# Kernel tuning notes

Hardware: AMD Instinct MI355X
Metric: run time of the kernel (lower is better)

Reference implementation:

```python
import jax, jax.numpy as jnp
import numpy as np

K = 3
PAD = 1
K2 = K * K


def _deform_conv(x, offset, w, b):
    """torchvision-style DeformConv2d, stride=1, padding=1, kernel=3, dilation=1.
    x: [B,C,H,W]; offset: [B,2*K2,H,W] (per-tap (dy,dx) interleaved); w: [O,C,K,K]; b: [O].
    """
    B, C, H, W = x.shape
    # kernel tap offsets relative to center (padding=1 => taps at -1,0,1)
    ky = (jnp.arange(K) - PAD).astype(x.dtype)
    kx = (jnp.arange(K) - PAD).astype(x.dtype)
    ky = jnp.repeat(ky, K)   # [K2]
    kx = jnp.tile(kx, K)     # [K2]

    off = offset.reshape(B, K2, 2, H, W)
    # sampling coordinates: [B,K2,H,W]
    yy = off[:, :, 0] + ky[None, :, None, None] + jnp.arange(H, dtype=x.dtype)[None, None, :, None]
    xx = off[:, :, 1] + kx[None, :, None, None] + jnp.arange(W, dtype=x.dtype)[None, None, None, :]

    def sample_one(img, yb, xb):  # img [C,H,W]; yb,xb [K2,H,W]
        y0 = jnp.floor(yb)
        x0 = jnp.floor(xb)
        dy = yb - y0
        dx = xb - x0
        y0i = y0.astype(jnp.int32)
        x0i = x0.astype(jnp.int32)
        img_flat = img.reshape(C, -1)

        def gather(yi, xi):
            valid = (yi >= 0) & (yi < H) & (xi >= 0) & (xi < W)
            idx = jnp.clip(yi, 0, H - 1) * W + jnp.clip(xi, 0, W - 1)
            v = jnp.take(img_flat, idx.reshape(-1), axis=1).reshape(C, K2, H, W)
            return v * valid[None].astype(img.dtype)

        v00 = gather(y0i, x0i)
        v01 = gather(y0i, x0i + 1)
        v10 = gather(y0i + 1, x0i)
        v11 = gather(y0i + 1, x0i + 1)
        w00 = ((1 - dy) * (1 - dx))[None]
        w01 = ((1 - dy) * dx)[None]
        w10 = (dy * (1 - dx))[None]
        w11 = (dy * dx)[None]
        return v00 * w00 + v01 * w01 + v10 * w10 + v11 * w11  # [C,K2,H,W]

    samp = jax.vmap(sample_one)(x, yy, xx)  # [B,C,K2,H,W]
    wr = w.reshape(w.shape[0], C, K2)       # [O,C,K2]
    out = jnp.einsum('bckhw,ock->bohw', samp, wr)
    return out + b[None, :, None, None]


def setup_inputs() -> dict:
    key = jax.random.key(0)
    ks = jax.random.split(key, 8)
    B, Cin, H, W = 16, 256, 32, 32
    Ch, NC = 256, 1000
    fan1 = Cin * K2
    fan2 = Ch * K2
    return {
        'x': jax.random.normal(ks[0], (B, Cin, H, W), jnp.float32),
        'offset': jax.random.normal(ks[1], (B, 2 * K2, H, W), jnp.float32),
        'w1': jax.random.normal(ks[2], (Ch, Cin, K, K), jnp.float32) / np.sqrt(fan1),
        'b1': jnp.zeros((Ch,), jnp.float32),
        'w2': jax.random.normal(ks[3], (Ch, Ch, K, K), jnp.float32) / np.sqrt(fan2),
        'b2': jnp.zeros((Ch,), jnp.float32),
        'fc_w': jax.random.normal(ks[4], (NC, Ch), jnp.float32) / np.sqrt(Ch),
        'fc_b': jnp.zeros((NC,), jnp.float32),
    }


def reference(x, offset, w1, b1, w2, b2, fc_w, fc_b):
    h = jax.nn.relu(_deform_conv(x, offset, w1, b1))
    h = jax.nn.relu(_deform_conv(h, offset, w2, b2))
    pooled = h.mean(axis=(2, 3))            # adaptive_avg_pool2d to (1,1) then flatten
    return pooled @ fc_w.T + fc_b
```

## Files before the change

kernel.cpp:

```cpp
#include <hip/hip_runtime.h>

#define B_   16
#define C_   256
#define H_   32
#define W_   32
#define O_   256
#define K2_  9
#define HW_  1024
#define KTOT 2304
#define NPOS 16384

typedef __bf16 bf16;
typedef __attribute__((ext_vector_type(8))) __bf16 bf16x8;
typedef __attribute__((ext_vector_type(4))) float  f32x4;

__device__ __forceinline__ void gload_lds16(const bf16* g, bf16* l) {
    __builtin_amdgcn_global_load_lds(
        (const __attribute__((address_space(1))) void*)g,
        (__attribute__((address_space(3))) void*)l, 16, 0, 0);
}

__device__ __forceinline__ float4 load4(const float* p, int t) {
    return ((const float4*)p)[t];
}
__device__ __forceinline__ float4 load4(const bf16* p, int t) {
    const ushort4 u = ((const ushort4*)p)[t];
    float4 f;
    f.x = __uint_as_float((unsigned)u.x << 16);
    f.y = __uint_as_float((unsigned)u.y << 16);
    f.z = __uint_as_float((unsigned)u.z << 16);
    f.w = __uint_as_float((unsigned)u.w << 16);
    return f;
}

__global__ __launch_bounds__(256) void prep_w(
    const float* __restrict__ w, bf16* __restrict__ Wm)
{
    const int o = blockIdx.x;
    for (int k = threadIdx.x; k < KTOT; k += 256) {
        const int cg  = k / 72;
        const int rem = k - cg * 72;
        const int tap = rem >> 3;
        const int cl  = rem & 7;
        const int c   = cg * 8 + cl;
        const int chunk  = cg * 9 + tap;
        const int chunkp = (chunk & ~7) | ((chunk ^ o) & 7);
        Wm[(size_t)o * KTOT + chunkp * 8 + cl] =
            (bf16)w[((size_t)o * C_ + c) * K2_ + tap];
    }
}

template<typename T>
__global__ __launch_bounds__(256) void sample_kernel(
    const T* __restrict__ src, size_t c_stride, size_t b_stride,
    const float* __restrict__ off,
    bf16* __restrict__ S)
{
    __shared__ ushort4 midx[576];
    __shared__ float4  mwgt[576];
    __shared__ float4  xs4[2][1152];

    const int tid = threadIdx.x;
    const int bx  = blockIdx.x;
    const int cg  = bx & 31;
    const int rt  = (bx >> 5) & 15;
    const int b   = bx >> 9;
    const int yrow = rt * 2;

    for (int item = tid; item < 576; item += 256) {
        const int pos = item & 63;
        const int k   = item >> 6;
        const int y   = yrow + (pos >> 5);
        const int x   = pos & 31;
        const float dyo = off[((b * 18 + 2 * k)     << 10) + (y << 5) + x];
        const float dxo = off[((b * 18 + 2 * k + 1) << 10) + (y << 5) + x];
        const float yy = dyo + (float)(k / 3 - 1) + (float)y;
        const float xx = dxo + (float)(k % 3 - 1) + (float)x;
        const float fy0 = floorf(yy), fx0 = floorf(xx);
        const float dy = yy - fy0, dx = xx - fx0;
        const int iy0 = (int)fy0, ix0 = (int)fx0;
        const int iy1 = iy0 + 1,  ix1 = ix0 + 1;
        const bool vy0 = (iy0 >= 0) && (iy0 < H_);
        const bool vy1 = (iy1 >= 0) && (iy1 < H_);
        const bool vx0 = (ix0 >= 0) && (ix0 < W_);
        const bool vx1 = (ix1 >= 0) && (ix1 < W_);
        const int cy0 = min(max(iy0, 0), H_ - 1), cy1 = min(max(iy1, 0), H_ - 1);
        const int cx0 = min(max(ix0, 0), W_ - 1), cx1 = min(max(ix1, 0), W_ - 1);
        ushort4 id; float4 wv;
        id.x = (unsigned short)(cy0 * W_ + cx0);
        wv.x = (vy0 && vx0) ? (1.f - dy) * (1.f - dx) : 0.f;
        id.y = (unsigned short)(cy0 * W_ + cx1);
        wv.y = (vy0 && vx1) ? (1.f - dy) * dx         : 0.f;
        id.z = (unsigned short)(cy1 * W_ + cx0);
        wv.z = (vy1 && vx0) ? dy * (1.f - dx)         : 0.f;
        id.w = (unsigned short)(cy1 * W_ + cx1);
        wv.w = (vy1 && vx1) ? dy * dx                 : 0.f;
        midx[item] = id;
        mwgt[item] = wv;
    }

    #pragma unroll
    for (int h = 0; h < 2; ++h) {
        const T* base = src + b * b_stride + (size_t)(cg * 8 + h * 4) * c_stride;
        const float4 v0 = load4(base,                tid);
        const float4 v1 = load4(base + c_stride,     tid);
        const float4 v2 = load4(base + 2 * c_stride, tid);
        const float4 v3 = load4(base + 3 * c_stride, tid);
        const int p0 = 4 * tid;
        xs4[h][(p0    ) + ((p0    ) >> 3)] = make_float4(v0.x, v1.x, v2.x, v3.x);
        xs4[h][(p0 + 1) + ((p0 + 1) >> 3)] = make_float4(v0.y, v1.y, v2.y, v3.y);
        xs4[h][(p0 + 2) + ((p0 + 2) >> 3)] = make_float4(v0.z, v1.z, v2.z, v3.z);
        xs4[h][(p0 + 3) + ((p0 + 3) >> 3)] = make_float4(v0.w, v1.w, v2.w, v3.w);
    }
    __syncthreads();

    for (int item = tid; item < 576; item += 256) {
        const int pos = item & 63;
        const int tap = item >> 6;
        const ushort4 id = midx[item];
        const float4  wv = mwgt[item];
        const int s0 = id.x + (id.x >> 3);
        const int s1 = id.y + (id.y >> 3);
        const int s2 = id.z + (id.z >> 3);
        const int s3 = id.w + (id.w >> 3);
        bf16x8 v;
        #pragma unroll
        for (int h = 0; h < 2; ++h) {
            const float4 a = xs4[h][s0], bb = xs4[h][s1];
            const float4 c = xs4[h][s2], d  = xs4[h][s3];
            v[h * 4 + 0] = (bf16)(wv.x * a.x + wv.y * bb.x + wv.z * c.x + wv.w * d.x);
            v[h * 4 + 1] = (bf16)(wv.x * a.y + wv.y * bb.y + wv.z * c.y + wv.w * d.y);
            v[h * 4 + 2] = (bf16)(wv.x * a.z + wv.y * bb.z + wv.z * c.z + wv.w * d.z);
            v[h * 4 + 3] = (bf16)(wv.x * a.w + wv.y * bb.w + wv.z * c.w + wv.w * d.w);
        }
        const int chunk  = cg * 9 + tap;
        const int chunkp = (chunk & ~7) | ((chunk ^ pos) & 7);
        *(bf16x8*)(S + (size_t)(b * 1024 + rt * 64 + pos) * KTOT + chunkp * 8) = v;
    }
}

template<bool POOL>
__global__ __launch_bounds__(256) void gemm_kernel(
    const bf16* __restrict__ A,
    const bf16* __restrict__ Bm,
    const float* __restrict__ bias,
    bf16* __restrict__ F,
    float* __restrict__ pooled)
{
    __shared__ bf16 Al[128 * 64];
    __shared__ bf16 Bl[64 * 64];

    const int tid  = threadIdx.x;
    const int om   = blockIdx.x >> 8;
    const int pn   = blockIdx.x & 255;
    const int wave = tid >> 6, lane = tid & 63;
    const int wr   = wave >> 1, wc = wave & 1;
    const int l15  = lane & 15, l4 = lane >> 4;

    f32x4 acc[4][2];
    #pragma unroll
    for (int m = 0; m < 4; ++m)
        #pragma unroll
        for (int n = 0; n < 2; ++n) acc[m][n] = (f32x4)0.f;

    for (int kt = 0; kt < KTOT / 64; ++kt) {
        __syncthreads();
        const int k0 = kt * 64;
        #pragma unroll
        for (int i = 0; i < 4; ++i) {
            const int flat = i * 256 + tid;
            const int rr = flat >> 3, kk = (flat & 7) << 3;
            gload_lds16(A + (size_t)(om * 128 + rr) * KTOT + k0 + kk,
                        &Al[(i * 256 + wave * 64) * 8]);
        }
        #pragma unroll
        for (int i = 0; i < 2; ++i) {
            const int flat = i * 256 + tid;
            const int rr = flat >> 3, kk = (flat & 7) << 3;
            gload_lds16(Bm + (size_t)(pn * 64 + rr) * KTOT + k0 + kk,
                        &Bl[(i * 256 + wave * 64) * 8]);
        }
        __syncthreads();

        #pragma unroll
        for (int ks = 0; ks < 2; ++ks) {
            const int cbase = ks * 4 + l4;
            bf16x8 af[4], bq[2];
            #pragma unroll
            for (int m = 0; m < 4; ++m) {
                const int R = wr * 64 + m * 16 + l15;
                af[m] = *(const bf16x8*)&Al[R * 64 + ((cbase ^ R) & 7) * 8];
            }
            #pragma unroll
            for (int n = 0; n < 2; ++n) {
                const int R = wc * 32 + n * 16 + l15;
                bq[n] = *(const bf16x8*)&Bl[R * 64 + ((cbase ^ R) & 7) * 8];
            }
            #pragma unroll
            for (int m = 0; m < 4; ++m)
                #pragma unroll
                for (int n = 0; n < 2; ++n)
                    acc[m][n] = __builtin_amdgcn_mfma_f32_16x16x32_bf16(
                        af[m], bq[n], acc[m][n], 0, 0, 0);
        }
    }

    const int obase = om * 128 + wr * 64;
    if (!POOL) {
        #pragma unroll
        for (int m = 0; m < 4; ++m)
            #pragma unroll
            for (int j = 0; j < 4; ++j) {
                const int o  = obase + m * 16 + l4 * 4 + j;
                const float bb = bias[o];
                #pragma unroll
                for (int n = 0; n < 2; ++n) {
                    const int col = pn * 64 + wc * 32 + n * 16 + l15;
                    F[(size_t)o * NPOS + col] =
                        (bf16)fmaxf(acc[m][n][j] + bb, 0.f);
                }
            }
    } else {
        const int b = pn >> 4;
        #pragma unroll
        for (int m = 0; m < 4; ++m)
            #pragma unroll
            for (int j = 0; j < 4; ++j) {
                const int o  = obase + m * 16 + l4 * 4 + j;
                const float bb = bias[o];
                float s = fmaxf(acc[m][0][j] + bb, 0.f) +
                          fmaxf(acc[m][1][j] + bb, 0.f);
                s += __shfl_xor(s, 1);
                s += __shfl_xor(s, 2);
                s += __shfl_xor(s, 4);
                s += __shfl_xor(s, 8);
                if (l15 == 0)
                    atomicAdd(&pooled[b * 256 + o], s * (1.f / 1024.f));
            }
    }
}

__global__ __launch_bounds__(256) void fc_kernel(
    const float* __restrict__ pooled, const float* __restrict__ fw,
    const float* __restrict__ fb, float* __restrict__ out)
{
    __shared__ float pl[C_];
    const int b = blockIdx.x >> 2;
    const int q = blockIdx.x & 3;
    const int t = threadIdx.x;
    pl[t] = pooled[b * C_ + t];
    __syncthreads();
    const int n = q * 250 + t;
    if (t < 250) {
        const float4* wr = (const float4*)(fw + (size_t)n * C_);
        float s = 0.f;
        #pragma unroll 8
        for (int j = 0; j < C_ / 4; ++j) {
            const float4 v = wr[j];
            s += v.x * pl[4 * j] + v.y * pl[4 * j + 1] +
                 v.z * pl[4 * j + 2] + v.w * pl[4 * j + 3];
        }
        out[b * 1000 + n] = s + fb[n];
    }
}

extern "C" void kernel_launch(void* const* d_in, const int* in_sizes, int n_in,
                              void* d_out, int out_size, void* d_ws, size_t ws_size,
                              hipStream_t stream)
{
    const float* x   = (const float*)d_in[0];
    const float* off = (const float*)d_in[1];
    const float* w1  = (const float*)d_in[2];
    const float* b1  = (const float*)d_in[3];
    const float* w2  = (const float*)d_in[4];
    const float* b2  = (const float*)d_in[5];
    const float* fcw = (const float*)d_in[6];
    const float* fcb = (const float*)d_in[7];
    float* outp = (float*)d_out;

    bf16*  S      = (bf16*)d_ws;
    bf16*  F2     = S + (size_t)NPOS * KTOT;
    bf16*  Wm1    = F2 + (size_t)O_ * NPOS;
    bf16*  Wm2    = Wm1 + (size_t)O_ * KTOT;
    float* pooled = (float*)(Wm2 + (size_t)O_ * KTOT);

    prep_w<<<O_, 256, 0, stream>>>(w1, Wm1);
    prep_w<<<O_, 256, 0, stream>>>(w2, Wm2);
    hipMemsetAsync(pooled, 0, B_ * O_ * sizeof(float), stream);

    sample_kernel<float><<<8192, 256, 0, stream>>>(
        x, (size_t)HW_, (size_t)C_ * HW_, off, S);
    gemm_kernel<false><<<512, 256, 0, stream>>>(Wm1, S, b1, F2, nullptr);

    sample_kernel<bf16><<<8192, 256, 0, stream>>>(
        F2, (size_t)NPOS, (size_t)HW_, off, S);
    gemm_kernel<true><<<512, 256, 0, stream>>>(Wm2, S, b2, nullptr, pooled);

    fc_kernel<<<B_ * 4, 256, 0, stream>>>(pooled, fcw, fcb, outp);
}
```

Before: 242.4 us.

## Use chunk-major tiled layouts for im2col and weights; sample four row tiles per block

The weight matrix and the sampled im2col buffer are now stored chunk-major within each GEMM tile. Each GEMM k-step therefore loads one contiguous 16KB/8KB block and reads LDS without XOR swizzling. The sampling kernel now covers four row tiles per block instead of one, so each 8-channel plane is staged in LDS once per four tiles. The bilinear index and weight computation moves inline, so it is recomputed per channel group rather than cached in LDS. The unswizzled LDS reads may cause bank conflicts, and the larger sample blocks lower the grid size and the available parallelism.

```diff
diff --git a/kernel.cpp b/kernel.cpp
--- a/kernel.cpp
+++ b/kernel.cpp
@@ -1,14 +1,16 @@
 #include <hip/hip_runtime.h>
 
-#define B_   16
-#define C_   256
-#define H_   32
-#define W_   32
-#define O_   256
-#define K2_  9
-#define HW_  1024
-#define KTOT 2304
-#define NPOS 16384
+#define B_     16
+#define C_     256
+#define H_     32
+#define W_     32
+#define O_     256
+#define K2_    9
+#define HW_    1024
+#define KTOT   2304
+#define NPOS   16384
+#define NCHUNK 288
+#define NT     256
 
 typedef __bf16 bf16;
 typedef __attribute__((ext_vector_type(8))) __bf16 bf16x8;
@@ -34,18 +36,18 @@
 }
 
 __global__ __launch_bounds__(256) void prep_w(
-    const float* __restrict__ w, bf16* __restrict__ Wm)
-{
-    const int o = blockIdx.x;
+    const float* __restrict__ w, bf16* __restrict__ Wt)
+{
+    const int o    = blockIdx.x;
+    const int om   = o >> 7, o128 = o & 127;
     for (int k = threadIdx.x; k < KTOT; k += 256) {
         const int cg  = k / 72;
         const int rem = k - cg * 72;
         const int tap = rem >> 3;
         const int cl  = rem & 7;
         const int c   = cg * 8 + cl;
-        const int chunk  = cg * 9 + tap;
-        const int chunkp = (chunk & ~7) | ((chunk ^ o) & 7);
-        Wm[(size_t)o * KTOT + chunkp * 8 + cl] =
+        const int chunk = cg * 9 + tap;
+        Wt[(((size_t)om * NCHUNK + chunk) * 128 + o128) * 8 + cl] =
             (bf16)w[((size_t)o * C_ + c) * K2_ + tap];
     }
 }
@@ -56,48 +58,12 @@
     const float* __restrict__ off,
     bf16* __restrict__ S)
 {
-    __shared__ ushort4 midx[576];
-    __shared__ float4  mwgt[576];
-    __shared__ float4  xs4[2][1152];
+    __shared__ float4 xs4[2][1152];
 
     const int tid = threadIdx.x;
-    const int bx  = blockIdx.x;
-    const int cg  = bx & 31;
-    const int rt  = (bx >> 5) & 15;
-    const int b   = bx >> 9;
-    const int yrow = rt * 2;
-
-    for (int item = tid; item < 576; item += 256) {
-        const int pos = item & 63;
-        const int k   = item >> 6;
-        const int y   = yrow + (pos >> 5);
-        const int x   = pos & 31;
-        const float dyo = off[((b * 18 + 2 * k)     << 10) + (y << 5) + x];
-        const float dxo = off[((b * 18 + 2 * k + 1) << 10) + (y << 5) + x];
-        const float yy = dyo + (float)(k / 3 - 1) + (float)y;
-        const float xx = dxo + (float)(k % 3 - 1) + (float)x;
-        const float fy0 = floorf(yy), fx0 = floorf(xx);
-        const float dy = yy - fy0, dx = xx - fx0;
-        const int iy0 = (int)fy0, ix0 = (int)fx0;
-        const int iy1 = iy0 + 1,  ix1 = ix0 + 1;
-        const bool vy0 = (iy0 >= 0) && (iy0 < H_);
-        const bool vy1 = (iy1 >= 0) && (iy1 < H_);
-        const bool vx0 = (ix0 >= 0) && (ix0 < W_);
-        const bool vx1 = (ix1 >= 0) && (ix1 < W_);
-        const int cy0 = min(max(iy0, 0), H_ - 1), cy1 = min(max(iy1, 0), H_ - 1);
-        const int cx0 = min(max(ix0, 0), W_ - 1), cx1 = min(max(ix1, 0), W_ - 1);
-        ushort4 id; float4 wv;
-        id.x = (unsigned short)(cy0 * W_ + cx0);
-        wv.x = (vy0 && vx0) ? (1.f - dy) * (1.f - dx) : 0.f;
-        id.y = (unsigned short)(cy0 * W_ + cx1);
-        wv.y = (vy0 && vx1) ? (1.f - dy) * dx         : 0.f;
-        id.z = (unsigned short)(cy1 * W_ + cx0);
-        wv.z = (vy1 && vx0) ? dy * (1.f - dx)         : 0.f;
-        id.w = (unsigned short)(cy1 * W_ + cx1);
-        wv.w = (vy1 && vx1) ? dy * dx                 : 0.f;
-        midx[item] = id;
-        mwgt[item] = wv;
-    }
+    const int cg  = blockIdx.x & 31;
+    const int rq  = (blockIdx.x >> 5) & 3;
+    const int b   = blockIdx.x >> 7;
 
     #pragma unroll
     for (int h = 0; h < 2; ++h) {
@@ -114,28 +80,52 @@
     }
     __syncthreads();
 
-    for (int item = tid; item < 576; item += 256) {
-        const int pos = item & 63;
-        const int tap = item >> 6;
-        const ushort4 id = midx[item];
-        const float4  wv = mwgt[item];
-        const int s0 = id.x + (id.x >> 3);
-        const int s1 = id.y + (id.y >> 3);
-        const int s2 = id.z + (id.z >> 3);
-        const int s3 = id.w + (id.w >> 3);
-        bf16x8 v;
-        #pragma unroll
-        for (int h = 0; h < 2; ++h) {
-            const float4 a = xs4[h][s0], bb = xs4[h][s1];
-            const float4 c = xs4[h][s2], d  = xs4[h][s3];
-            v[h * 4 + 0] = (bf16)(wv.x * a.x + wv.y * bb.x + wv.z * c.x + wv.w * d.x);
-            v[h * 4 + 1] = (bf16)(wv.x * a.y + wv.y * bb.y + wv.z * c.y + wv.w * d.y);
-            v[h * 4 + 2] = (bf16)(wv.x * a.z + wv.y * bb.z + wv.z * c.z + wv.w * d.z);
-            v[h * 4 + 3] = (bf16)(wv.x * a.w + wv.y * bb.w + wv.z * c.w + wv.w * d.w);
+    for (int i = 0; i < 4; ++i) {
+        const int rt   = rq * 4 + i;
+        const int yrow = rt * 2;
+        const int t    = b * 16 + rt;
+        for (int item = tid; item < 576; item += 256) {
+            const int pos = item & 63;
+            const int tap = item >> 6;
+            const int y   = yrow + (pos >> 5);
+            const int x   = pos & 31;
+            const float dyo = off[((b * 18 + 2 * tap)     << 10) + (y << 5) + x];
+            const float dxo = off[((b * 18 + 2 * tap + 1) << 10) + (y << 5) + x];
+            const float yy = dyo + (float)(tap / 3 - 1) + (float)y;
+            const float xx = dxo + (float)(tap % 3 - 1) + (float)x;
+            const float fy0 = floorf(yy), fx0 = floorf(xx);
+            const float dy = yy - fy0, dx = xx - fx0;
+            const int iy0 = (int)fy0, ix0 = (int)fx0;
+            const int iy1 = iy0 + 1,  ix1 = ix0 + 1;
+            const bool vy0 = (iy0 >= 0) && (iy0 < H_);
+            const bool vy1 = (iy1 >= 0) && (iy1 < H_);
+            const bool vx0 = (ix0 >= 0) && (ix0 < W_);
+            const bool vx1 = (ix1 >= 0) && (ix1 < W_);
+            const int cy0 = min(max(iy0, 0), H_ - 1), cy1 = min(max(iy1, 0), H_ - 1);
+            const int cx0 = min(max(ix0, 0), W_ - 1), cx1 = min(max(ix1, 0), W_ - 1);
+            const int p00 = cy0 * W_ + cx0, p01 = cy0 * W_ + cx1;
+            const int p10 = cy1 * W_ + cx0, p11 = cy1 * W_ + cx1;
+            const float w00 = (vy0 && vx0) ? (1.f - dy) * (1.f - dx) : 0.f;
+            const float w01 = (vy0 && vx1) ? (1.f - dy) * dx         : 0.f;
+            const float w10 = (vy1 && vx0) ? dy * (1.f - dx)         : 0.f;
+            const float w11 = (vy1 && vx1) ? dy * dx                 : 0.f;
+            const int s0 = p00 + (p00 >> 3);
+            const int s1 = p01 + (p01 >> 3);
+            const int s2 = p10 + (p10 >> 3);
+            const int s3 = p11 + (p11 >> 3);
+            bf16x8 v;
+            #pragma unroll
+            for (int h = 0; h < 2; ++h) {
+                const float4 a = xs4[h][s0], bb = xs4[h][s1];
+                const float4 c = xs4[h][s2], d  = xs4[h][s3];
+                v[h * 4 + 0] = (bf16)(w00 * a.x + w01 * bb.x + w10 * c.x + w11 * d.x);
+                v[h * 4 + 1] = (bf16)(w00 * a.y + w01 * bb.y + w10 * c.y + w11 * d.y);
+                v[h * 4 + 2] = (bf16)(w00 * a.z + w01 * bb.z + w10 * c.z + w11 * d.z);
+                v[h * 4 + 3] = (bf16)(w00 * a.w + w01 * bb.w + w10 * c.w + w11 * d.w);
+            }
+            const int chunk = cg * 9 + tap;
+            *(bf16x8*)(S + (((size_t)t * NCHUNK + chunk) * 64 + pos) * 8) = v;
         }
-        const int chunk  = cg * 9 + tap;
-        const int chunkp = (chunk & ~7) | ((chunk ^ pos) & 7);
-        *(bf16x8*)(S + (size_t)(b * 1024 + rt * 64 + pos) * KTOT + chunkp * 8) = v;
     }
 }
 
@@ -147,8 +137,8 @@
     bf16* __restrict__ F,
     float* __restrict__ pooled)
 {
-    __shared__ bf16 Al[128 * 64];
-    __shared__ bf16 Bl[64 * 64];
+    __shared__ bf16 Al[8192];
+    __shared__ bf16 Bl[4096];
 
     const int tid  = threadIdx.x;
     const int om   = blockIdx.x >> 8;
@@ -157,44 +147,40 @@
     const int wr   = wave >> 1, wc = wave & 1;
     const int l15  = lane & 15, l4 = lane >> 4;
 
+    const bf16* Abase = A  + (size_t)om * NCHUNK * 128 * 8;
+    const bf16* Bbase = Bm + (size_t)pn * NCHUNK * 64 * 8;
+
     f32x4 acc[4][2];
     #pragma unroll
     for (int m = 0; m < 4; ++m)
         #pragma unroll
         for (int n = 0; n < 2; ++n) acc[m][n] = (f32x4)0.f;
 
-    for (int kt = 0; kt < KTOT / 64; ++kt) {
+    for (int kt = 0; kt < NCHUNK / 8; ++kt) {
         __syncthreads();
-        const int k0 = kt * 64;
-        #pragma unroll
-        for (int i = 0; i < 4; ++i) {
-            const int flat = i * 256 + tid;
-            const int rr = flat >> 3, kk = (flat & 7) << 3;
-            gload_lds16(A + (size_t)(om * 128 + rr) * KTOT + k0 + kk,
+        #pragma unroll
+        for (int i = 0; i < 4; ++i)
+            gload_lds16(Abase + (size_t)kt * 8192 + (i * 256 + tid) * 8,
                         &Al[(i * 256 + wave * 64) * 8]);
-        }
-        #pragma unroll
-        for (int i = 0; i < 2; ++i) {
-            const int flat = i * 256 + tid;
-            const int rr = flat >> 3, kk = (flat & 7) << 3;
-            gload_lds16(Bm + (size_t)(pn * 64 + rr) * KTOT + k0 + kk,
+        #pragma unroll
+        for (int i = 0; i < 2; ++i)
+            gload_lds16(Bbase + (size_t)kt * 4096 + (i * 256 + tid) * 8,
                         &Bl[(i * 256 + wave * 64) * 8]);
-        }
         __syncthreads();
 
         #pragma unroll
         for (int ks = 0; ks < 2; ++ks) {
-            const int cbase = ks * 4 + l4;
+            const int cb = ks * 4 + l4;
             bf16x8 af[4], bq[2];
             #pragma unroll
             for (int m = 0; m < 4; ++m) {
                 const int R = wr * 64 + m * 16 + l15;
-                af[m] = *(const bf16x8*)&Al[R * 64 + ((cbase ^ R) & 7) * 8];
+                af[m] = *(const bf16x8*)&Al[(cb * 128 + R) * 8];
             }
             #pragma unroll
             for (int n = 0; n < 2; ++n) {
                 const int R = wc * 32 + n * 16 + l15;
-                bq[n] = *(const bf16x8*)&Bl[R * 64 + ((cbase ^ R) & 7) * 8];
+                bq[n] = *(const bf16x8*)&Bl[(cb * 64 + R) * 8];
             }
             #pragma unroll
             for (int m = 0; m < 4; ++m)
@@ -280,21 +266,21 @@
 
     bf16*  S      = (bf16*)d_ws;
     bf16*  F2     = S + (size_t)NPOS * KTOT;
-    bf16*  Wm1    = F2 + (size_t)O_ * NPOS;
-    bf16*  Wm2    = Wm1 + (size_t)O_ * KTOT;
-    float* pooled = (float*)(Wm2 + (size_t)O_ * KTOT);
-
-    prep_w<<<O_, 256, 0, stream>>>(w1, Wm1);
-    prep_w<<<O_, 256, 0, stream>>>(w2, Wm2);
+    bf16*  Wt1    = F2 + (size_t)O_ * NPOS;
+    bf16*  Wt2    = Wt1 + (size_t)O_ * KTOT;
+    float* pooled = (float*)(Wt2 + (size_t)O_ * KTOT);
+
+    prep_w<<<O_, 256, 0, stream>>>(w1, Wt1);
+    prep_w<<<O_, 256, 0, stream>>>(w2, Wt2);
     hipMemsetAsync(pooled, 0, B_ * O_ * sizeof(float), stream);
 
-    sample_kernel<float><<<8192, 256, 0, stream>>>(
+    sample_kernel<float><<<2048, 256, 0, stream>>>(
         x, (size_t)HW_, (size_t)C_ * HW_, off, S);
-    gemm_kernel<false><<<512, 256, 0, stream>>>(Wm1, S, b1, F2, nullptr);
-
-    sample_kernel<bf16><<<8192, 256, 0, stream>>>(
+    gemm_kernel<false><<<512, 256, 0, stream>>>(Wt1, S, b1, F2, nullptr);
+
+    sample_kernel<bf16><<<2048, 256, 0, stream>>>(
         F2, (size_t)NPOS, (size_t)HW_, off, S);
-    gemm_kernel<true><<<512, 256, 0, stream>>>(Wm2, S, b2, nullptr, pooled);
+    gemm_kernel<true><<<512, 256, 0, stream>>>(Wt2, S, b2, nullptr, pooled);
 
     fc_kernel<<<B_ * 4, 256, 0, stream>>>(pooled, fcw, fcb, outp);
 }
```

New measurement: 207.5 us. 14.4% less time.
